# Kernel optimization log

Measured on AMD Instinct MI355X. Metric: run time of the kernel, lower is better.

The kernel has to match this reference:

```python
import jax, jax.numpy as jnp
import numpy as np

NUM_EMBEDDINGS = 2048
EMBEDDING_DIM = 256
COMMITMENT_COST = 0.25


def setup_inputs() -> dict:
    key = jax.random.key(0)
    k1, k2 = jax.random.split(key)
    inputs = jax.random.normal(k1, (2, EMBEDDING_DIM, 24, 24, 24), dtype=jnp.float32)
    embedding_weight = jax.random.normal(k2, (NUM_EMBEDDINGS, EMBEDDING_DIM), dtype=jnp.float32)
    return {"inputs": inputs, "embedding_weight": embedding_weight}


def reference(inputs, embedding_weight):
    # [B, C, D, H, W] -> [B, D, H, W, C]
    x = jnp.transpose(inputs, (0, 2, 3, 4, 1))
    in_shape = x.shape
    flat = x.reshape(-1, EMBEDDING_DIM)  # [N, D]

    distances = (
        jnp.sum(flat * flat, axis=1, keepdims=True)
        + jnp.sum(embedding_weight * embedding_weight, axis=1)
        - 2.0 * flat @ embedding_weight.T
    )
    encoding_indices = jnp.argmin(distances, axis=1)  # [N]
    encodings = jax.nn.one_hot(encoding_indices, NUM_EMBEDDINGS, dtype=jnp.float32)  # [N, K]

    # Gather instead of one_hot @ W (same math, no redundant GEMM)
    quantized = embedding_weight[encoding_indices].reshape(in_shape)

    e_latent_loss = jnp.mean((jax.lax.stop_gradient(quantized) - x) ** 2)
    loss = COMMITMENT_COST * e_latent_loss

    # Straight-through estimator
    quantized_st = x + jax.lax.stop_gradient(quantized - x)

    avg_probs = jnp.mean(encodings, axis=0)
    perplexity = jnp.exp(-jnp.sum(avg_probs * jnp.log(avg_probs + 1e-10)))

    quantized_out = jnp.transpose(quantized_st, (0, 4, 1, 2, 3))
    return (loss, quantized_out, perplexity, encodings, encoding_indices[:, None])
```

## Files before the change

kernel.cpp:

```cpp
#include <hip/hip_runtime.h>

#define S_SP   13824
#define CHAN   256
#define NQ     27648
#define KCODES 2048
#define CS     3538944
#define OFF_Q   1
#define OFF_PPL 7077889
#define OFF_ENC 7077890LL
#define OFF_IDX 63700994LL

typedef __bf16 bf16x8 __attribute__((ext_vector_type(8)));
typedef float  f32x4  __attribute__((ext_vector_type(4)));

#define GLOAD_LDS16(g, s)                                                      \
  __builtin_amdgcn_global_load_lds(                                            \
      (const __attribute__((address_space(1))) void*)(g),                      \
      (__attribute__((address_space(3))) void*)(s), 16, 0, 0)

__device__ __forceinline__ unsigned int f2bf(float f) {
  unsigned int u = __float_as_uint(f);
  unsigned int r = u + 0x7FFFu + ((u >> 16) & 1u);
  return r >> 16;
}
__device__ __forceinline__ float bf2f(unsigned int h) {
  return __uint_as_float(h << 16);
}
__device__ __forceinline__ void fsplit(float f, unsigned int& hi, unsigned int& lo) {
  hi = f2bf(f);
  float r = f - bf2f(hi);
  lo = f2bf(r);
}

__global__ __launch_bounds__(256) void prep_w(const float* __restrict__ W,
                                              unsigned short* __restrict__ Wh,
                                              unsigned short* __restrict__ Wl,
                                              float* __restrict__ wn) {
  int g = blockIdx.x * 256 + threadIdx.x;
  int row = g >> 5;
  int d0 = (g & 31) * 8;
  const float* Wp = W + (size_t)row * CHAN + d0;
  float v[8];
  *(float4*)(v) = *(const float4*)Wp;
  *(float4*)(v + 4) = *(const float4*)(Wp + 4);
  float s = 0.f;
  unsigned int h[8], l[8];
#pragma unroll
  for (int j = 0; j < 8; ++j) {
    s = fmaf(v[j], v[j], s);
    fsplit(v[j], h[j], l[j]);
  }
  int4 ph, pl;
  ph.x = (int)(h[0] | (h[1] << 16)); ph.y = (int)(h[2] | (h[3] << 16));
  ph.z = (int)(h[4] | (h[5] << 16)); ph.w = (int)(h[6] | (h[7] << 16));
  pl.x = (int)(l[0] | (l[1] << 16)); pl.y = (int)(l[2] | (l[3] << 16));
  pl.z = (int)(l[4] | (l[5] << 16)); pl.w = (int)(l[6] | (l[7] << 16));
  *(int4*)(Wh + (size_t)row * CHAN + d0) = ph;
  *(int4*)(Wl + (size_t)row * CHAN + d0) = pl;
  for (int off = 16; off; off >>= 1) s += __shfl_down(s, off);
  if ((threadIdx.x & 31) == 0) wn[row] = s;
}

__global__ __launch_bounds__(256) void prep_x(const float* __restrict__ X,
                                              unsigned short* __restrict__ Xh,
                                              unsigned short* __restrict__ Xl) {
  __shared__ float xs[32 * 257];
  int t = threadIdx.x;
  int qb = blockIdx.x * 32;
  int b = qb / S_SP, s0 = qb % S_SP;
  const float* xp = X + (size_t)b * CS + s0;
  int q = t & 31;
  int db = t >> 5;
  for (int r = 0; r < 32; ++r) {
    int d = db + (r << 3);
    xs[q * 257 + d] = xp[(size_t)d * S_SP + q];
  }
  __syncthreads();
  int row = t >> 3, c8 = t & 7;
  size_t obase = (size_t)(qb + row) * CHAN;
  const float* rp0 = xs + row * 257;
#pragma unroll
  for (int j = 0; j < 4; ++j) {
    int d = j * 64 + c8 * 8;
    const float* rp = rp0 + d;
    unsigned int h[8], l[8];
#pragma unroll
    for (int e = 0; e < 8; ++e) fsplit(rp[e], h[e], l[e]);
    int4 ph, pl;
    ph.x = (int)(h[0] | (h[1] << 16)); ph.y = (int)(h[2] | (h[3] << 16));
    ph.z = (int)(h[4] | (h[5] << 16)); ph.w = (int)(h[6] | (h[7] << 16));
    pl.x = (int)(l[0] | (l[1] << 16)); pl.y = (int)(l[2] | (l[3] << 16));
    pl.z = (int)(l[4] | (l[5] << 16)); pl.w = (int)(l[6] | (l[7] << 16));
    *(int4*)(Xh + obase + d) = ph;
    *(int4*)(Xl + obase + d) = pl;
  }
}

__global__ __launch_bounds__(256, 2) void dist_mfma(const unsigned short* __restrict__ Xh,
                                                    const unsigned short* __restrict__ Xl,
                                                    const unsigned short* __restrict__ Wh,
                                                    const unsigned short* __restrict__ Wl,
                                                    const float* __restrict__ wn,
                                                    float* __restrict__ rB1,
                                                    int* __restrict__ rI1,
                                                    float* __restrict__ rB2) {
  __shared__ __align__(16) unsigned short sW[2][2][4096];
  __shared__ float wnl[1024];
  int t = threadIdx.x;
  int w = t >> 6, l = t & 63;
  int lr = l & 15, lc = l >> 4;
  int kg = blockIdx.x & 1;
  int qb = (blockIdx.x >> 1) * 128;
  int kofs = kg << 10;

  for (int j = t; j < 1024; j += 256) wnl[j] = wn[kofs + j];

  bf16x8 ah[2][8], al[2][8];
#pragma unroll
  for (int s = 0; s < 2; ++s) {
    size_t base = (size_t)(qb + w * 32 + s * 16 + lr) * CHAN + lc * 8;
#pragma unroll
    for (int c = 0; c < 8; ++c) {
      ah[s][c] = *(const bf16x8*)(Xh + base + c * 32);
      al[s][c] = *(const bf16x8*)(Xl + base + c * 32);
    }
  }

  float b1[2][4], b2[2][4]; int i1[2][4];
#pragma unroll
  for (int s = 0; s < 2; ++s)
#pragma unroll
    for (int r = 0; r < 4; ++r) { b1[s][r] = 3.4e38f; b2[s][r] = 3.4e38f; i1[s][r] = 0; }

  auto stage = [&](int buf, int kt) {
    size_t rb = (size_t)(kofs + (kt << 4) + lr) * CHAN + lc * 8;
    GLOAD_LDS16(Wh + rb + w * 32,        &sW[buf][0][w * 512]);
    GLOAD_LDS16(Wh + rb + (w + 4) * 32,  &sW[buf][0][(w + 4) * 512]);
    GLOAD_LDS16(Wl + rb + w * 32,        &sW[buf][1][w * 512]);
    GLOAD_LDS16(Wl + rb + (w + 4) * 32,  &sW[buf][1][(w + 4) * 512]);
  };

  stage(0, 0);
  __syncthreads();

  for (int kt = 0; kt < 64; ++kt) {
    int cur = kt & 1;
    if (kt < 63) stage(cur ^ 1, kt + 1);
    f32x4 a0 = {0.f, 0.f, 0.f, 0.f}, a1 = {0.f, 0.f, 0.f, 0.f};
#pragma unroll
    for (int c = 0; c < 8; ++c) {
      bf16x8 bh = *(const bf16x8*)&sW[cur][0][c * 512 + (l << 3)];
      bf16x8 bl = *(const bf16x8*)&sW[cur][1][c * 512 + (l << 3)];
      a0 = __builtin_amdgcn_mfma_f32_16x16x32_bf16(ah[0][c], bh, a0, 0, 0, 0);
      a1 = __builtin_amdgcn_mfma_f32_16x16x32_bf16(ah[1][c], bh, a1, 0, 0, 0);
      a0 = __builtin_amdgcn_mfma_f32_16x16x32_bf16(al[0][c], bh, a0, 0, 0, 0);
      a1 = __builtin_amdgcn_mfma_f32_16x16x32_bf16(al[1][c], bh, a1, 0, 0, 0);
      a0 = __builtin_amdgcn_mfma_f32_16x16x32_bf16(ah[0][c], bl, a0, 0, 0, 0);
      a1 = __builtin_amdgcn_mfma_f32_16x16x32_bf16(ah[1][c], bl, a1, 0, 0, 0);
    }
    int k = kofs + (kt << 4) + lr;
    float wnk = wnl[(kt << 4) + lr];
#pragma unroll
    for (int r = 0; r < 4; ++r) {
      float s0 = fmaf(-2.0f, a0[r], wnk);
      bool lt0 = s0 < b1[0][r];
      b2[0][r] = fminf(b2[0][r], fmaxf(s0, b1[0][r]));
      b1[0][r] = lt0 ? s0 : b1[0][r];
      i1[0][r] = lt0 ? k : i1[0][r];
      float s1 = fmaf(-2.0f, a1[r], wnk);
      bool lt1 = s1 < b1[1][r];
      b2[1][r] = fminf(b2[1][r], fmaxf(s1, b1[1][r]));
      b1[1][r] = lt1 ? s1 : b1[1][r];
      i1[1][r] = lt1 ? k : i1[1][r];
    }
    __syncthreads();
  }

#pragma unroll
  for (int m = 1; m < 16; m <<= 1) {
#pragma unroll
    for (int s = 0; s < 2; ++s)
#pragma unroll
      for (int r = 0; r < 4; ++r) {
        float ob1 = __shfl_xor(b1[s][r], m);
        int   oi  = __shfl_xor(i1[s][r], m);
        float ob2 = __shfl_xor(b2[s][r], m);
        bool sw = (ob1 < b1[s][r]) || (ob1 == b1[s][r] && oi < i1[s][r]);
        b2[s][r] = fminf(fmaxf(b1[s][r], ob1), fminf(b2[s][r], ob2));
        b1[s][r] = sw ? ob1 : b1[s][r];
        i1[s][r] = sw ? oi : i1[s][r];
      }
  }
  if (lr == 0) {
#pragma unroll
    for (int s = 0; s < 2; ++s)
#pragma unroll
      for (int r = 0; r < 4; ++r) {
        int q = qb + w * 32 + s * 16 + lc * 4 + r;
        size_t o = (size_t)kg * NQ + q;
        rB1[o] = b1[s][r]; rI1[o] = i1[s][r]; rB2[o] = b2[s][r];
      }
  }
}

__global__ __launch_bounds__(256) void merge_k(const float* __restrict__ rB1,
                                               const int* __restrict__ rI1,
                                               const float* __restrict__ rB2,
                                               float* __restrict__ idx_out,
                                               int* __restrict__ flagcount,
                                               int* __restrict__ flaglist) {
  int n = blockIdx.x * 256 + threadIdx.x;
  float B1 = rB1[n]; int I1 = rI1[n]; float B2 = rB2[n];
  float c1 = rB1[NQ + n]; int ci = rI1[NQ + n]; float c2 = rB2[NQ + n];
  bool sw = (c1 < B1) || (c1 == B1 && ci < I1);
  float nb2 = fminf(fmaxf(B1, c1), fminf(B2, c2));
  float nb1 = sw ? c1 : B1;
  int   ni  = sw ? ci : I1;
  if (nb2 - nb1 < 0.05f) {
    int slot = atomicAdd(flagcount, 1);
    flaglist[slot] = n;
    idx_out[n] = 0.0f;
  } else {
    idx_out[n] = (float)ni;
  }
}

__global__ __launch_bounds__(256) void refine2(const float* __restrict__ X,
                                               const float* __restrict__ W,
                                               const int* __restrict__ flagcount,
                                               const int* __restrict__ flaglist,
                                               float* __restrict__ idx_out) {
  __shared__ double xd[CHAN];
  __shared__ double rv[256];
  __shared__ int    ri[256];
  int t = threadIdx.x;
  int cnt = flagcount[0];
  for (int j = blockIdx.x; j < cnt; j += gridDim.x) {
    __syncthreads();
    int n = flaglist[j];
    int b = n / S_SP, s = n % S_SP;
    xd[t] = (double)X[(size_t)b * CS + (size_t)t * S_SP + s];
    __syncthreads();

    double best = 1e300;
    int bi = 1 << 30;
    for (int jj = 0; jj < 8; ++jj) {
      int k = t * 8 + jj;
      const float* Wp = W + (size_t)k * CHAN;
      double dsum = 0.0;
      for (int d = 0; d < CHAN; ++d) {
        double df = xd[d] - (double)Wp[d];
        dsum = fma(df, df, dsum);
      }
      if (dsum < best) { best = dsum; bi = k; }
    }
    rv[t] = best; ri[t] = bi;
    __syncthreads();
    for (int off = 128; off > 0; off >>= 1) {
      if (t < off) {
        if (rv[t + off] < rv[t] || (rv[t + off] == rv[t] && ri[t + off] < ri[t])) {
          rv[t] = rv[t + off]; ri[t] = ri[t + off];
        }
      }
      __syncthreads();
    }
    if (t == 0) idx_out[n] = (float)ri[0];
  }
}

__global__ __launch_bounds__(256) void scatter_stats(const float* __restrict__ X,
                                                     const float* __restrict__ W,
                                                     float* __restrict__ outF,
                                                     int* __restrict__ counts,
                                                     float* __restrict__ loss_acc) {
  __shared__ int h[KCODES];
  __shared__ float wred[4];
  int t = threadIdx.x;
  for (int j = t; j < KCODES; j += 256) h[j] = 0;
  __syncthreads();

  int n = blockIdx.x * 256 + t;
  int idx = (int)outF[OFF_IDX + n];
  atomicAdd(&h[idx], 1);
  outF[OFF_ENC + (size_t)n * KCODES + idx] = 1.0f;

  int b = n / S_SP, s = n % S_SP;
  const float* Wp = W + (size_t)idx * CHAN;
  const float* xp = X + (size_t)b * CS + s;
  float* qp = outF + OFF_Q + (size_t)b * CS + s;

  float lsum = 0.f;
#pragma unroll 4
  for (int c = 0; c < CHAN; ++c) {
    float wv = Wp[c];
    float xv = xp[(size_t)c * S_SP];
    qp[(size_t)c * S_SP] = wv;
    float df = wv - xv;
    lsum = fmaf(df, df, lsum);
  }

  for (int off = 32; off; off >>= 1) lsum += __shfl_down(lsum, off);
  if ((t & 63) == 0) wred[t >> 6] = lsum;
  __syncthreads();
  if (t == 0) atomicAdd(loss_acc, wred[0] + wred[1] + wred[2] + wred[3]);

  for (int j = t; j < KCODES; j += 256) {
    int v = h[j];
    if (v) atomicAdd(&counts[j], v);
  }
}

__global__ __launch_bounds__(256) void finalize(const int* __restrict__ counts,
                                                const float* __restrict__ loss_acc,
                                                float* __restrict__ outF) {
  __shared__ double red[256];
  int t = threadIdx.x;
  double H = 0.0;
  for (int k = t; k < KCODES; k += 256) {
    double p = (double)counts[k] / (double)NQ;
    H += p * log(p + 1e-10);
  }
  red[t] = H;
  __syncthreads();
  for (int off = 128; off > 0; off >>= 1) {
    if (t < off) red[t] += red[t + off];
    __syncthreads();
  }
  if (t == 0) {
    outF[0] = 0.25f * (loss_acc[0] / 7077888.0f);
    outF[OFF_PPL] = (float)exp(-red[0]);
  }
}

extern "C" void kernel_launch(void* const* d_in, const int* in_sizes, int n_in,
                              void* d_out, int out_size, void* d_ws, size_t ws_size,
                              hipStream_t stream) {
  const float* X = (const float*)d_in[0];
  const float* W = (const float*)d_in[1];
  float* outF = (float*)d_out;
  char* ws = (char*)d_ws;
  float* wn        = (float*)ws;
  int*   counts    = (int*)(ws + 8192);
  float* loss_acc  = (float*)(ws + 16384);
  int*   flagcount = (int*)(ws + 16388);
  int*   flaglist  = (int*)(ws + 20480);
  float* rB1       = (float*)(ws + 131072);
  int*   rI1       = (int*)(ws + 360448);
  float* rB2       = (float*)(ws + 589824);
  unsigned short* Wh = (unsigned short*)(ws + 1048576);
  unsigned short* Wl = (unsigned short*)(ws + 2097152);
  unsigned short* Xh = (unsigned short*)(ws + 3145728);
  unsigned short* Xl = Xh + (size_t)NQ * CHAN;

  hipMemsetAsync(ws + 8192, 0, 8208, stream);
  hipMemsetAsync((char*)d_out + OFF_ENC * 4, 0, (size_t)NQ * KCODES * 4, stream);

  prep_w<<<256, 256, 0, stream>>>(W, Wh, Wl, wn);
  prep_x<<<NQ / 32, 256, 0, stream>>>(X, Xh, Xl);
  dist_mfma<<<(NQ / 128) * 2, 256, 0, stream>>>(Xh, Xl, Wh, Wl, wn, rB1, rI1, rB2);
  merge_k<<<NQ / 256, 256, 0, stream>>>(rB1, rI1, rB2, outF + OFF_IDX, flagcount, flaglist);
  refine2<<<256, 256, 0, stream>>>(X, W, flagcount, flaglist, outF + OFF_IDX);
  scatter_stats<<<NQ / 256, 256, 0, stream>>>(X, W, outF, counts, loss_acc);
  finalize<<<1, 256, 0, stream>>>(counts, loss_acc, outF);
}
```

Before: 273.7 us.

## Fuse one-hot encoding write into merge kernel and drop separate memset

Removes the separate memset of the 226 MB one-hot encodings buffer. The merge kernel now writes each full one-hot row itself with nontemporal 8-byte stores, using one 32-thread group per row, and the refine kernel patches rows whose index changes. Scatter_stats is restructured to 64 points per block with four channel groups, and it uses global atomics for counts in place of a shared histogram. This saves one full pass over the encoding buffer and the later scattered stores, at the cost of more global atomics on counts and a larger workspace for the flag list.

```diff
diff --git a/kernel.cpp b/kernel.cpp
--- a/kernel.cpp
+++ b/kernel.cpp
@@ -203,49 +203,64 @@
   }
 }
 
-__global__ __launch_bounds__(256) void merge_k(const float* __restrict__ rB1,
-                                               const int* __restrict__ rI1,
-                                               const float* __restrict__ rB2,
-                                               float* __restrict__ idx_out,
-                                               int* __restrict__ flagcount,
-                                               int* __restrict__ flaglist) {
-  int n = blockIdx.x * 256 + threadIdx.x;
+__global__ __launch_bounds__(256) void merge_emit(const float* __restrict__ rB1,
+                                                  const int* __restrict__ rI1,
+                                                  const float* __restrict__ rB2,
+                                                  float* __restrict__ outF,
+                                                  int* __restrict__ flagcount,
+                                                  int2* __restrict__ flaglist) {
+  int t = threadIdx.x;
+  int r = t >> 5, j = t & 31;
+  int n = blockIdx.x * 8 + r;
+
   float B1 = rB1[n]; int I1 = rI1[n]; float B2 = rB2[n];
   float c1 = rB1[NQ + n]; int ci = rI1[NQ + n]; float c2 = rB2[NQ + n];
   bool sw = (c1 < B1) || (c1 == B1 && ci < I1);
   float nb2 = fminf(fmaxf(B1, c1), fminf(B2, c2));
   float nb1 = sw ? c1 : B1;
   int   ni  = sw ? ci : I1;
-  if (nb2 - nb1 < 0.05f) {
-    int slot = atomicAdd(flagcount, 1);
-    flaglist[slot] = n;
-    idx_out[n] = 0.0f;
-  } else {
-    idx_out[n] = (float)ni;
+
+  if (j == 0) {
+    if (nb2 - nb1 < 0.05f) {
+      int slot = atomicAdd(flagcount, 1);
+      flaglist[slot] = make_int2(n, ni);
+    }
+    outF[OFF_IDX + n] = (float)ni;
+  }
+
+  float* row = outF + OFF_ENC + (size_t)n * KCODES;
+#pragma unroll
+  for (int k = 0; k < 32; ++k) {
+    int col = 2 * j + 64 * k;
+    union { float f[2]; unsigned long long u; } v;
+    v.f[0] = (col == ni) ? 1.0f : 0.0f;
+    v.f[1] = (col + 1 == ni) ? 1.0f : 0.0f;
+    __builtin_nontemporal_store(v.u, (unsigned long long*)(row + col));
   }
 }
 
 __global__ __launch_bounds__(256) void refine2(const float* __restrict__ X,
                                                const float* __restrict__ W,
                                                const int* __restrict__ flagcount,
-                                               const int* __restrict__ flaglist,
-                                               float* __restrict__ idx_out) {
+                                               const int2* __restrict__ flaglist,
+                                               float* __restrict__ outF) {
   __shared__ double xd[CHAN];
   __shared__ double rv[256];
   __shared__ int    ri[256];
   int t = threadIdx.x;
   int cnt = flagcount[0];
-  for (int j = blockIdx.x; j < cnt; j += gridDim.x) {
-    __syncthreads();
-    int n = flaglist[j];
+  for (int jj = blockIdx.x; jj < cnt; jj += gridDim.x) {
+    __syncthreads();
+    int2 e = flaglist[jj];
+    int n = e.x, prov = e.y;
     int b = n / S_SP, s = n % S_SP;
     xd[t] = (double)X[(size_t)b * CS + (size_t)t * S_SP + s];
     __syncthreads();
 
     double best = 1e300;
     int bi = 1 << 30;
-    for (int jj = 0; jj < 8; ++jj) {
-      int k = t * 8 + jj;
+    for (int j8 = 0; j8 < 8; ++j8) {
+      int k = t * 8 + j8;
       const float* Wp = W + (size_t)k * CHAN;
       double dsum = 0.0;
       for (int d = 0; d < CHAN; ++d) {
@@ -264,7 +279,15 @@
       }
       __syncthreads();
     }
-    if (t == 0) idx_out[n] = (float)ri[0];
+    if (t == 0) {
+      int fin = ri[0];
+      outF[OFF_IDX + n] = (float)fin;
+      if (fin != prov) {
+        float* row = outF + OFF_ENC + (size_t)n * KCODES;
+        row[prov] = 0.0f;
+        row[fin]  = 1.0f;
+      }
+    }
   }
 }
 
@@ -273,25 +296,27 @@
                                                      float* __restrict__ outF,
                                                      int* __restrict__ counts,
                                                      float* __restrict__ loss_acc) {
-  __shared__ int h[KCODES];
+  __shared__ int sidx[64];
   __shared__ float wred[4];
   int t = threadIdx.x;
-  for (int j = t; j < KCODES; j += 256) h[j] = 0;
-  __syncthreads();
-
-  int n = blockIdx.x * 256 + t;
-  int idx = (int)outF[OFF_IDX + n];
-  atomicAdd(&h[idx], 1);
-  outF[OFF_ENC + (size_t)n * KCODES + idx] = 1.0f;
-
+  int q = t & 63, cg = t >> 6;
+  int n = blockIdx.x * 64 + q;
+  if (t < 64) {
+    int idx = (int)outF[OFF_IDX + n];
+    sidx[t] = idx;
+    atomicAdd(&counts[idx], 1);
+  }
+  __syncthreads();
+  int idx = sidx[q];
   int b = n / S_SP, s = n % S_SP;
   const float* Wp = W + (size_t)idx * CHAN;
   const float* xp = X + (size_t)b * CS + s;
   float* qp = outF + OFF_Q + (size_t)b * CS + s;
 
   float lsum = 0.f;
-#pragma unroll 4
-  for (int c = 0; c < CHAN; ++c) {
+#pragma unroll 8
+  for (int k = 0; k < 64; ++k) {
+    int c = cg + (k << 2);
     float wv = Wp[c];
     float xv = xp[(size_t)c * S_SP];
     qp[(size_t)c * S_SP] = wv;
@@ -303,11 +328,6 @@
   if ((t & 63) == 0) wred[t >> 6] = lsum;
   __syncthreads();
   if (t == 0) atomicAdd(loss_acc, wred[0] + wred[1] + wred[2] + wred[3]);
-
-  for (int j = t; j < KCODES; j += 256) {
-    int v = h[j];
-    if (v) atomicAdd(&counts[j], v);
-  }
 }
 
 __global__ __launch_bounds__(256) void finalize(const int* __restrict__ counts,
@@ -343,23 +363,22 @@
   int*   counts    = (int*)(ws + 8192);
   float* loss_acc  = (float*)(ws + 16384);
   int*   flagcount = (int*)(ws + 16388);
-  int*   flaglist  = (int*)(ws + 20480);
-  float* rB1       = (float*)(ws + 131072);
-  int*   rI1       = (int*)(ws + 360448);
-  float* rB2       = (float*)(ws + 589824);
+  int2*  flaglist  = (int2*)(ws + 32768);
+  float* rB1       = (float*)(ws + 262144);
+  int*   rI1       = (int*)(ws + 483328);
+  float* rB2       = (float*)(ws + 704512);
   unsigned short* Wh = (unsigned short*)(ws + 1048576);
   unsigned short* Wl = (unsigned short*)(ws + 2097152);
   unsigned short* Xh = (unsigned short*)(ws + 3145728);
   unsigned short* Xl = Xh + (size_t)NQ * CHAN;
 
-  hipMemsetAsync(ws + 8192, 0, 8208, stream);
-  hipMemsetAsync((char*)d_out + OFF_ENC * 4, 0, (size_t)NQ * KCODES * 4, stream);
+  hipMemsetAsync(ws + 8192, 0, 8200, stream);
 
   prep_w<<<256, 256, 0, stream>>>(W, Wh, Wl, wn);
   prep_x<<<NQ / 32, 256, 0, stream>>>(X, Xh, Xl);
   dist_mfma<<<(NQ / 128) * 2, 256, 0, stream>>>(Xh, Xl, Wh, Wl, wn, rB1, rI1, rB2);
-  merge_k<<<NQ / 256, 256, 0, stream>>>(rB1, rI1, rB2, outF + OFF_IDX, flagcount, flaglist);
-  refine2<<<256, 256, 0, stream>>>(X, W, flagcount, flaglist, outF + OFF_IDX);
-  scatter_stats<<<NQ / 256, 256, 0, stream>>>(X, W, outF, counts, loss_acc);
+  merge_emit<<<NQ / 8, 256, 0, stream>>>(rB1, rI1, rB2, outF, flagcount, flaglist);
+  refine2<<<256, 256, 0, stream>>>(X, W, flagcount, flaglist, outF);
+  scatter_stats<<<NQ / 64, 256, 0, stream>>>(X, W, outF, counts, loss_acc);
   finalize<<<1, 256, 0, stream>>>(counts, loss_acc, outF);
 }
```

New measurement: 268.5 us. Within noise of the previous version (-1.9%).
